# Optimization experiments

Measured on AMD Instinct MI355X. Metric: run time of the kernel, lower is better.

Reference implementation:

```python
import math
import jax, jax.numpy as jnp
import numpy as np

EMBED_DIM = 1024
ZDIM = 128
CHUNK = 2048
DSTATE = 16
DT_RANK = math.ceil(EMBED_DIM / 16)  # 64


def silu(x):
    return x * jax.nn.sigmoid(x)


def rmsnorm(x, w, eps=1e-5):
    var = jnp.mean(x * x, axis=-1, keepdims=True)
    return x * jax.lax.rsqrt(var + eps) * w


def _rotary(v, sin, cos):
    # v: (n, d) -> rotate half
    x1, x2 = jnp.split(v, 2, axis=-1)
    return jnp.concatenate([x1 * cos - x2 * sin, x2 * cos + x1 * sin], axis=-1)


def rel_pos_bias(alpha, beta, n):
    half = ZDIM // 2
    freqs = jnp.exp(jnp.arange(half, dtype=jnp.float32) * (-math.log(10000.0) / half))
    ang = jnp.arange(n, dtype=jnp.float32)[:, None] * freqs[None, :]
    sin, cos = jnp.sin(ang), jnp.cos(ang)
    a = _rotary(jnp.broadcast_to(alpha, (n, ZDIM)), sin, cos)
    b = _rotary(jnp.broadcast_to(beta, (n, ZDIM)), sin, cos)
    return jnp.einsum('mk,nk->mn', a, b)


def s6(u, xproj_w, dt_w, dt_b, A_log, D_p):
    # Mamba-style selective scan. u: (B, L, D)
    x_dbl = u @ xproj_w.T  # (B,L,dt_rank+2*N)
    dt, Bm, Cm = jnp.split(x_dbl, [DT_RANK, DT_RANK + DSTATE], axis=-1)
    dt = jax.nn.softplus(dt @ dt_w.T + dt_b)  # (B,L,D)
    A = -jnp.exp(A_log)  # (D,N)

    def step(h, inp):
        dt_t, B_t, C_t, u_t = inp  # (B,D),(B,N),(B,N),(B,D)
        dA = jnp.exp(dt_t[..., None] * A)  # (B,D,N)
        h = dA * h + (dt_t * u_t)[..., None] * B_t[:, None, :]
        y = jnp.einsum('bdn,bn->bd', h, C_t)
        return h, y

    B, L, D = u.shape
    h0 = jnp.zeros((B, D, DSTATE), u.dtype)
    xs = (dt.transpose(1, 0, 2), Bm.transpose(1, 0, 2), Cm.transpose(1, 0, 2), u.transpose(1, 0, 2))
    _, ys = jax.lax.scan(step, h0, xs)  # ys: (L,B,D)
    return ys.transpose(1, 0, 2) + u * D_p


def setup_inputs() -> dict:
    key = jax.random.key(0)
    ks = jax.random.split(key, 12)
    std = 0.02
    B, L, D = 2, 4096, EMBED_DIM
    f32 = jnp.float32
    inp = {
        'x': jax.random.normal(ks[0], (B, L, D), f32),
        'norm_w': jnp.ones((D,), f32),
        'v_w': jax.random.normal(ks[1], (D, D), f32) * std,
        'v_b': jnp.zeros((D,), f32),
        'mx_w': jax.random.normal(ks[2], (ZDIM + D + 2 * D, D), f32) * std,
        'mx_b': jnp.zeros((ZDIM + 3 * D,), f32),
        'h_w': jax.random.normal(ks[3], (D, D), f32) * std,
        'h_b': jnp.zeros((D,), f32),
        'gamma': jax.random.normal(ks[4], (2, ZDIM), f32) * std,
        'beta': jnp.zeros((2, ZDIM), f32),
        'alpha_rb': jax.random.normal(ks[5], (1, ZDIM), f32) * std,
        'beta_rb': jax.random.normal(ks[6], (1, ZDIM), f32) * std,
        'xproj_w': jax.random.normal(ks[7], (DT_RANK + 2 * DSTATE, D), f32) * std,
        'dt_w': jax.random.normal(ks[8], (D, DT_RANK), f32) * std,
        'dt_b': jnp.full((D,), -4.6, f32),  # softplus -> dt ~ 0.01
        'A_log': jnp.log(jnp.broadcast_to(jnp.arange(1, DSTATE + 1, dtype=f32), (D, DSTATE))),
        'D_p': jnp.ones((D,), f32),
    }
    return inp


def reference(x, norm_w, v_w, v_b, mx_w, mx_b, h_w, h_b, gamma, beta,
              alpha_rb, beta_rb, xproj_w, dt_w, dt_b, A_log, D_p):
    B, L, D = x.shape
    residual = x
    xn = rmsnorm(x, norm_w)
    v = silu(xn @ v_w.T + v_b)                       # (B,L,hdim)
    mx = silu(s6(xn, xproj_w, dt_w, dt_b, A_log, D_p))
    base = mx @ mx_w.T + mx_b                        # (B,L,zdim+hdim+2D)
    u, zr, hx = jnp.split(base, [D, D + ZDIM + D], axis=-1)
    u = jax.nn.sigmoid(u)
    zr = silu(zr)
    z, r = jnp.split(zr, [ZDIM], axis=-1)
    z = z[..., None, :] * gamma + beta               # (B,L,2,Z)
    q, k = z[..., 0, :], z[..., 1, :]
    c = min(CHUNK, L)
    nc = L // c
    qh = q.reshape(B, nc, c, ZDIM) * (ZDIM ** -0.5)
    kh = k.reshape(B, nc, c, ZDIM)
    vh = v.reshape(B, nc, c, D)
    bias = rel_pos_bias(alpha_rb, beta_rb, c)        # (c,c)
    mask = jnp.triu(jnp.full((c, c), -jnp.inf, jnp.float32), 1)
    qk = jnp.einsum('bnqz,bnkz->bnqk', qh, kh) + bias + mask
    attn = jax.nn.softmax(qk.astype(jnp.float32), axis=-1).astype(qk.dtype)
    h = jnp.einsum('bnqk,bnkd->bnqd', attn, vh).reshape(B, L, D)
    h = silu(hx + (h * r) @ h_w.T + h_b)
    return residual + u * (h - residual)
```

## Files before the change

### kernel.cpp

```cpp
#include <hip/hip_runtime.h>
#include <hip/hip_bf16.h>
#include <math.h>

#define EMBED 1024
#define LSEQ 4096
#define BATCH 2
#define ZD 128
#define CHUNKC 2048
#define NSTATE 16
#define DTR 64
#define XDBL_W 96
#define NSEG 64
#define TSEG 64

typedef __attribute__((ext_vector_type(8))) short bf16x8;
typedef __attribute__((ext_vector_type(4))) float f32x4;

__device__ __forceinline__ float sigmoidf_(float x){ return 1.f/(1.f+__expf(-x)); }
__device__ __forceinline__ float siluf_(float x){ return x/(1.f+__expf(-x)); }
__device__ __forceinline__ __hip_bfloat16 tobf(float x){ return __float2bfloat16(x); }
__device__ __forceinline__ float frombf(__hip_bfloat16 x){ return __bfloat162float(x); }

__device__ __forceinline__ void gload_lds16(const void* g, void* l) {
  __builtin_amdgcn_global_load_lds(
      (const __attribute__((address_space(1))) unsigned int*)g,
      (__attribute__((address_space(3))) unsigned int*)l, 16, 0, 0);
}

__global__ __launch_bounds__(256) void prep_k(
    const float* __restrict__ v_w, const float* __restrict__ xproj_w,
    const float* __restrict__ h_w, const float* __restrict__ dt_w,
    const float* __restrict__ mx_w,
    const float* __restrict__ alpha, const float* __restrict__ beta,
    __hip_bfloat16* __restrict__ wcat, __hip_bfloat16* __restrict__ hwb,
    __hip_bfloat16* __restrict__ dtwb, __hip_bfloat16* __restrict__ mxwb,
    float* __restrict__ gtab)
{
  int b = blockIdx.x, tid = threadIdx.x;
  if (b < 5440) {
    const float* s; __hip_bfloat16* d; int idx;
    if (b < 1024)      { idx = (b*256+tid)*4;        s = v_w + idx;      d = wcat + idx; }
    else if (b < 1120) { idx = ((b-1024)*256+tid)*4; s = xproj_w + idx;  d = wcat + (1<<20) + idx; }
    else if (b < 1152) { idx = ((b-1120)*256+tid)*4; s = nullptr;        d = wcat + (1<<20) + 96*1024 + idx; }
    else if (b < 2176) { idx = ((b-1152)*256+tid)*4; s = h_w + idx;      d = hwb + idx; }
    else if (b < 2240) { idx = ((b-2176)*256+tid)*4; s = dt_w + idx;     d = dtwb + idx; }
    else               { idx = ((b-2240)*256+tid)*4; s = mx_w + idx;     d = mxwb + idx; }
    if (s) {
      float4 v = *(const float4*)s;
      d[0]=tobf(v.x); d[1]=tobf(v.y); d[2]=tobf(v.z); d[3]=tobf(v.w);
    } else {
      d[0]=tobf(0.f); d[1]=tobf(0.f); d[2]=tobf(0.f); d[3]=tobf(0.f);
    }
    return;
  }
  __shared__ float P[64], Q[64], F[64];
  if (tid < 64) {
    float a1=alpha[tid], a2=alpha[64+tid], b1=beta[tid], b2=beta[64+tid];
    P[tid]=a1*b1+a2*b2;
    Q[tid]=a2*b1-a1*b2;
    F[tid]=expf(-0.14391156831f*(float)tid);
  }
  __syncthreads();
  int d = (b-5440)*256 + tid;
  if (d < CHUNKC) {
    float s=0.f;
    for (int j=0;j<64;++j){
      float th = (float)d * F[j];
      float sn, cs;
      sincosf(th, &sn, &cs);
      s += P[j]*cs - Q[j]*sn;
    }
    gtab[d]=s;
  }
}

__global__ __launch_bounds__(256) void rmsnorm_k(const float* __restrict__ x,
                                                 const float* __restrict__ w,
                                                 __hip_bfloat16* __restrict__ xnb) {
  size_t row = blockIdx.x;
  const float* px = x + row*EMBED;
  int tid = threadIdx.x;
  float4 xv = *(const float4*)(px + tid*4);
  float ss = xv.x*xv.x + xv.y*xv.y + xv.z*xv.z + xv.w*xv.w;
  #pragma unroll
  for (int off=32; off; off>>=1) ss += __shfl_down(ss, off, 64);
  __shared__ float red[4];
  if ((tid&63)==0) red[tid>>6]=ss;
  __syncthreads();
  float tot = red[0]+red[1]+red[2]+red[3];
  float scale = rsqrtf(tot*(1.f/EMBED) + 1e-5f);
  float4 wv = *(const float4*)(w + tid*4);
  __hip_bfloat16* pb = xnb + row*EMBED + tid*4;
  pb[0]=tobf(xv.x*scale*wv.x); pb[1]=tobf(xv.y*scale*wv.y);
  pb[2]=tobf(xv.z*scale*wv.z); pb[3]=tobf(xv.w*scale*wv.w);
}

template<bool FINAL>
__global__ __launch_bounds__(256) void seg_scan_k(
    const float* __restrict__ xbc,
    const __hip_bfloat16* __restrict__ dtv,
    const __hip_bfloat16* __restrict__ xnu,
    const float* __restrict__ A_log,
    const float* __restrict__ D_p,
    const float* __restrict__ segInit,
    float* __restrict__ segP,
    float* __restrict__ segH,
    __hip_bfloat16* __restrict__ mx)
{
  int bx = blockIdx.x;
  int seg = bx >> 3;
  int grp = bx & 7;
  int b = grp >> 2;
  int d = (grp & 3)*256 + threadIdx.x;
  int ch = b*EMBED + d;
  int tid = threadIdx.x;
  int tbase = seg*TSEG;

  float A[NSTATE], h[NSTATE], P[NSTATE];
  #pragma unroll
  for (int n=0;n<NSTATE;++n){
    A[n] = -__expf(A_log[(size_t)d*NSTATE+n]);
    P[n] = 1.f;
  }
  if (FINAL) {
    const float* si = segInit + ((size_t)seg*2048 + ch)*NSTATE;
    #pragma unroll
    for (int n=0;n<NSTATE;++n) h[n] = si[n];
  } else {
    #pragma unroll
    for (int n=0;n<NSTATE;++n) h[n] = 0.f;
  }
  float Dp = FINAL ? D_p[d] : 0.f;

  __shared__ float BCb[8][32];
  const float* xd = xbc + ((size_t)b*LSEQ + tbase)*32;
  const __hip_bfloat16* pdt = dtv + ((size_t)b*LSEQ + tbase)*EMBED + d;
  const __hip_bfloat16* pu  = xnu + ((size_t)b*LSEQ + tbase)*EMBED + d;
  __hip_bfloat16* pmx = mx + ((size_t)b*LSEQ + tbase)*EMBED + d;

  for (int t0=0; t0<TSEG; t0+=8) {
    __syncthreads();
    { int tt = tid>>5, jj = tid&31;
      BCb[tt][jj] = xd[(size_t)(t0+tt)*32 + jj]; }
    __syncthreads();
    #pragma unroll
    for (int tt=0; tt<8; ++tt) {
      int t = t0 + tt;
      float dtt = frombf(pdt[(size_t)t*EMBED]);
      float ut  = frombf(pu[(size_t)t*EMBED]);
      float du = dtt*ut;
      float y = 0.f;
      #pragma unroll
      for (int n=0;n<NSTATE;++n){
        float dA = __expf(dtt*A[n]);
        h[n] = dA*h[n] + du*BCb[tt][n];
        if (!FINAL) P[n] *= dA;
        if (FINAL)  y += h[n]*BCb[tt][16+n];
      }
      if (FINAL) pmx[(size_t)t*EMBED] = tobf(siluf_(y + ut*Dp));
    }
  }
  if (!FINAL) {
    float* pp = segP + ((size_t)seg*2048 + ch)*NSTATE;
    float* ph = segH + ((size_t)seg*2048 + ch)*NSTATE;
    #pragma unroll
    for (int n=0;n<NSTATE;n+=4){
      *(float4*)(pp+n) = make_float4(P[n],P[n+1],P[n+2],P[n+3]);
      *(float4*)(ph+n) = make_float4(h[n],h[n+1],h[n+2],h[n+3]);
    }
  }
}

__global__ __launch_bounds__(256) void seg_combine_k(const float* __restrict__ segP,
                                                     const float* __restrict__ segH,
                                                     float* __restrict__ segInit) {
  int idx = blockIdx.x*256 + threadIdx.x;
  float H = 0.f;
  for (int s=0; s<NSEG; ++s) {
    size_t o = (size_t)s*32768 + idx;
    float Pv = segP[o], hl = segH[o];
    segInit[o] = H;
    H = Pv*H + hl;
  }
}

__global__ __launch_bounds__(256) void softmax_k(const __hip_bfloat16* __restrict__ S,
                                                 __hip_bfloat16* __restrict__ Sb) {
  size_t row = blockIdx.x;
  const __hip_bfloat16* p = S + row*CHUNKC;
  __hip_bfloat16* po = Sb + row*CHUNKC;
  int tid = threadIdx.x;
  int r = (int)(row & (CHUNKC-1));
  int nb = (r >> 8) + 1;
  int kcl = ((r >> 7) + 1) << 7;
  float v[8];
  float m = -1e30f;
  #pragma unroll
  for (int i=0;i<8;++i){
    if (i < nb) {
      float t = frombf(p[tid + i*256]);
      v[i] = (i*256 + tid <= r) ? t : -1e30f;
    } else v[i] = -1e30f;
    m = fmaxf(m, v[i]);
  }
  #pragma unroll
  for (int off=32; off; off>>=1) m = fmaxf(m, __shfl_down(m, off, 64));
  __shared__ float red[4];
  if ((tid&63)==0) red[tid>>6]=m;
  __syncthreads();
  m = fmaxf(fmaxf(red[0],red[1]),fmaxf(red[2],red[3]));
  float s=0.f;
  #pragma unroll
  for (int i=0;i<8;++i){ v[i]=__expf(v[i]-m); s+=v[i]; }
  #pragma unroll
  for (int off=32; off; off>>=1) s += __shfl_down(s, off, 64);
  __syncthreads();
  if ((tid&63)==0) red[tid>>6]=s;
  __syncthreads();
  s = red[0]+red[1]+red[2]+red[3];
  float inv = 1.f/s;
  #pragma unroll
  for (int i=0;i<8;++i){
    int c = tid + i*256;
    if (c < kcl) po[c] = tobf(v[i]*inv);
  }
}

__global__ __launch_bounds__(256) void transpose_k(const unsigned short* __restrict__ vb,
                                                   unsigned short* __restrict__ VT) {
  __shared__ unsigned short t[64][68];
  int tid = threadIdx.x;
  int tr = tid>>4;
  int tc = (tid&15)*4;
  int c0 = blockIdx.x*64, r0 = blockIdx.y*64;
  #pragma unroll
  for (int it=0; it<4; ++it) {
    int r = it*16 + tr;
    ushort4 v = *(const ushort4*)(vb + (size_t)(r0+r)*EMBED + c0 + tc);
    t[r][tc+0]=v.x; t[r][tc+1]=v.y; t[r][tc+2]=v.z; t[r][tc+3]=v.w;
  }
  __syncthreads();
  int ch = r0 >> 11;
  int kb = r0 & 2047;
  #pragma unroll
  for (int it=0; it<4; ++it) {
    int nl = it*16 + tr;
    ushort4 o;
    o.x = t[tc+0][nl]; o.y = t[tc+1][nl]; o.z = t[tc+2][nl]; o.w = t[tc+3][nl];
    *(ushort4*)(VT + ((size_t)ch*EMBED + c0 + nl)*CHUNKC + kb + tc) = o;
  }
}

struct MEp {
  const float* bias; const float* gtab; const float* gamma; const float* beta2;
  __hip_bfloat16* ug; __hip_bfloat16* qo; __hip_bfloat16* ko; __hip_bfloat16* ro; __hip_bfloat16* hxo;
  const __hip_bfloat16* rb; const __hip_bfloat16* hxb; const __hip_bfloat16* ub;
  const float* resid; float* outp;
  __hip_bfloat16* Cb; int ldc;
  float* f32o; __hip_bfloat16* bf16o;
};

__device__ __forceinline__ void xcd_swz(int& bx, int& by) {
  const int gx = gridDim.x;
  const int nwg = gx*gridDim.y;
  const int lin = by*gx + bx;
  const int qq = nwg >> 3, rr = nwg & 7;
  const int xcd = lin & 7, pos = lin >> 3;
  const int base = (xcd < rr) ? xcd*(qq+1) : rr*(qq+1) + (xcd-rr)*qq;
  const int lg = base + pos;
  bx = lg % gx; by = lg / gx;
}

#define MBM 128
#define MBK 64

template<int EPI, bool TRIK, bool SWZ>
__global__ __launch_bounds__(256, 4) void mgemm_k(
    const __hip_bfloat16* __restrict__ A, int lda, long long sAz,
    const __hip_bfloat16* __restrict__ B, int ldb, long long sBz,
    int K, MEp ep)
{
  __shared__ __attribute__((aligned(16))) short As[MBM*MBK];
  __shared__ __attribute__((aligned(16))) short Bs[MBM*MBK];
  const int tid = threadIdx.x;
  const int wv = tid>>6, lane = tid&63;
  const int z = blockIdx.z;
  A += (size_t)z * sAz;
  B += (size_t)z * sBz;
  int bx = blockIdx.x, by = blockIdx.y;
  if constexpr (SWZ) xcd_swz(bx, by);
  const int m0 = by*MBM, n0 = bx*MBM;
  if constexpr (EPI==2) { if (n0 > m0 + (MBM-1)) return; }
  const int r8 = lane>>3, g8 = lane&7;
  const int csrc = g8 ^ r8;
  const int wr = wv>>1, wc = wv&1;
  const int fr = lane&15, qv = lane>>4;
  const int x7 = fr & 7;

  int Ktot = K;
  if constexpr (TRIK) { int km = m0 + MBM; Ktot = km < K ? km : K; }
  const int nt = Ktot / MBK;

  f32x4 acc[4][4] = {};

  const __hip_bfloat16* Ag = A + (size_t)(m0 + wv*32 + r8)*lda + csrc*8;
  const __hip_bfloat16* Bg = B + (size_t)(n0 + wv*32 + r8)*ldb + csrc*8;

  auto stage = [&](int t){
    const int k0 = t*MBK;
    short* Al = &As[wv*32*MBK];
    short* Bl = &Bs[wv*32*MBK];
    #pragma unroll
    for (int j=0;j<4;++j)
      gload_lds16(Ag + (size_t)(j*8)*lda + k0, Al + j*8*MBK);
    #pragma unroll
    for (int j=0;j<4;++j)
      gload_lds16(Bg + (size_t)(j*8)*ldb + k0, Bl + j*8*MBK);
  };

  for (int t=0; t<nt; ++t) {
    stage(t);
    __syncthreads();
    #pragma unroll
    for (int kk=0; kk<2; ++kk) {
      const int pos8 = ((kk*4 + qv) ^ x7) * 8;
      bf16x8 af[4], bfr[4];
      #pragma unroll
      for (int mi=0;mi<4;++mi)
        af[mi] = *(const bf16x8*)&As[(wr*64 + mi*16 + fr)*MBK + pos8];
      #pragma unroll
      for (int ni=0;ni<4;++ni)
        bfr[ni] = *(const bf16x8*)&Bs[(wc*64 + ni*16 + fr)*MBK + pos8];
      #pragma unroll
      for (int mi=0;mi<4;++mi)
        #pragma unroll
        for (int ni=0;ni<4;++ni)
          acc[mi][ni] = __builtin_amdgcn_mfma_f32_16x16x32_bf16(af[mi], bfr[ni], acc[mi][ni], 0,0,0);
    }
    if (t+1 < nt) __syncthreads();
  }

  const int vr = (lane>>4)*4;
  #pragma unroll
  for (int mi=0;mi<4;++mi) {
    #pragma unroll
    for (int v=0; v<4; ++v) {
      const int row = m0 + wr*64 + mi*16 + vr + v;
      #pragma unroll
      for (int ni=0;ni<4;++ni) {
        const int col = n0 + wc*64 + ni*16 + fr;
        float val = acc[mi][ni][v];
        if constexpr (EPI==1) {
          val += ep.bias[col];
          if (col < 1024) {
            ep.ug[(size_t)row*EMBED + col] = tobf(sigmoidf_(val));
          } else if (col < 1152) {
            int jj = col - 1024;
            float zz = siluf_(val);
            ep.qo[(size_t)row*ZD + jj] = tobf((zz*ep.gamma[jj] + ep.beta2[jj]) * 0.08838834764831845f);
            ep.ko[(size_t)row*ZD + jj] = tobf(zz*ep.gamma[128+jj] + ep.beta2[128+jj]);
          } else if (col < 2176) {
            ep.ro[(size_t)row*EMBED + (col-1152)] = tobf(siluf_(val));
          } else {
            ep.hxo[(size_t)row*EMBED + (col-2176)] = tobf(val);
          }
        } else if constexpr (EPI==2) {
          __hip_bfloat16* Sp = ep.Cb + (size_t)z*CHUNKC*CHUNKC;
          if (col <= row) Sp[(size_t)row*CHUNKC + col] = tobf(val + ep.gtab[row-col]);
        } else if constexpr (EPI==3) {
          size_t gr = (size_t)z*CHUNKC + row;
          ep.Cb[gr*EMBED + col] = tobf(val * frombf(ep.rb[gr*EMBED + col]));
        } else if constexpr (EPI==4) {
          float zz = val + ep.bias[col] + frombf(ep.hxb[(size_t)row*EMBED + col]);
          float hh = siluf_(zz);
          float res = ep.resid[(size_t)row*EMBED + col];
          ep.outp[(size_t)row*EMBED + col] = res + frombf(ep.ub[(size_t)row*EMBED + col])*(hh-res);
        } else if constexpr (EPI==6) {
          float zv = val + ep.bias[col];
          ep.bf16o[(size_t)row*EMBED + col] = tobf((zv > 15.f) ? zv : log1pf(__expf(zv)));
        } else {
          if (col < 1024) {
            ep.Cb[(size_t)row*ep.ldc + col] = tobf(siluf_(val + ep.bias[col]));
          } else {
            int jj = col - 1024;
            if (jj < DTR)          ep.bf16o[(size_t)row*DTR + jj] = tobf(val);
            else if (jj < XDBL_W)  ep.f32o[(size_t)row*32 + (jj - DTR)] = val;
          }
        }
      }
    }
  }
}

extern "C" void kernel_launch(void* const* d_in, const int* in_sizes, int n_in,
                              void* d_out, int out_size, void* d_ws, size_t ws_size,
                              hipStream_t stream) {
  const float* x       = (const float*)d_in[0];
  const float* norm_w  = (const float*)d_in[1];
  const float* v_w     = (const float*)d_in[2];
  const float* v_b     = (const float*)d_in[3];
  const float* mx_w    = (const float*)d_in[4];
  const float* mx_b    = (const float*)d_in[5];
  const float* h_w     = (const float*)d_in[6];
  const float* h_b     = (const float*)d_in[7];
  const float* gamma   = (const float*)d_in[8];
  const float* beta    = (const float*)d_in[9];
  const float* alpha_rb= (const float*)d_in[10];
  const float* beta_rb = (const float*)d_in[11];
  const float* xproj_w = (const float*)d_in[12];
  const float* dt_w    = (const float*)d_in[13];
  const float* dt_b    = (const float*)d_in[14];
  const float* A_log   = (const float*)d_in[15];
  const float* D_p     = (const float*)d_in[16];
  float* out = (float*)d_out;

  float* ws = (float*)d_ws;
  size_t off = 0;
  auto alloc = [&](size_t n){ float* p = ws + off; off += n; return p; };
  const size_t BL2 = (size_t)BATCH*LSEQ;

  float* sbzone  = alloc(BL2*EMBED);
  float* scratch = alloc((size_t)2*CHUNKC*CHUNKC*2);
  float* xbc     = alloc(BL2*32);
  float* gtab    = alloc(CHUNKC);
  auto balloc = [&](size_t nbf){ __hip_bfloat16* p = (__hip_bfloat16*)(ws + off); off += (nbf+1)/2; return p; };
  __hip_bfloat16* xnb   = balloc(BL2*EMBED);
  __hip_bfloat16* vbufb = balloc(BL2*EMBED);
  __hip_bfloat16* mxb   = balloc(BL2*EMBED);
  __hip_bfloat16* qb    = balloc(BL2*ZD);
  __hip_bfloat16* kb    = balloc(BL2*ZD);
  __hip_bfloat16* ugb   = balloc(BL2*EMBED);
  __hip_bfloat16* rbb   = balloc(BL2*EMBED);
  __hip_bfloat16* hxbb  = balloc(BL2*EMBED);
  __hip_bfloat16* hrb   = balloc(BL2*EMBED);
  __hip_bfloat16* xdblb = balloc(BL2*DTR);
  __hip_bfloat16* wcat  = balloc((size_t)1152*EMBED);
  __hip_bfloat16* mxwb  = balloc((size_t)3200*EMBED);
  __hip_bfloat16* hwb   = balloc((size_t)EMBED*EMBED);
  __hip_bfloat16* dtwb  = balloc((size_t)EMBED*DTR);

  __hip_bfloat16* dtbb = (__hip_bfloat16*)scratch;
  float* segP    = scratch + BL2*EMBED;
  float* segH    = segP + (size_t)NSEG*2048*NSTATE;
  float* segInit = segH + (size_t)NSEG*2048*NSTATE;
  __hip_bfloat16* S  = (__hip_bfloat16*)scratch;
  __hip_bfloat16* Sb = (__hip_bfloat16*)sbzone;
  __hip_bfloat16* VT = xnb;

  prep_k<<<5448, 256, 0, stream>>>(v_w, xproj_w, h_w, dt_w, mx_w,
                                   alpha_rb, beta_rb,
                                   wcat, hwb, dtwb, mxwb, gtab);

  rmsnorm_k<<<(int)BL2, 256, 0, stream>>>(x, norm_w, xnb);

  MEp ep;

  ep = {}; ep.bias = v_b; ep.Cb = vbufb; ep.ldc = EMBED;
  ep.f32o = xbc; ep.bf16o = xdblb;
  mgemm_k<7,false,true><<<dim3(1152/MBM, BL2/MBM), 256, 0, stream>>>(
      xnb, EMBED, 0, wcat, EMBED, 0, EMBED, ep);

  ep = {}; ep.bias = dt_b; ep.bf16o = dtbb;
  mgemm_k<6,false,true><<<dim3(EMBED/MBM, BL2/MBM), 256, 0, stream>>>(
      xdblb, DTR, 0, dtwb, DTR, 0, DTR, ep);

  seg_scan_k<false><<<NSEG*8, 256, 0, stream>>>(xbc, dtbb, xnb, A_log, D_p,
                                                nullptr, segP, segH, nullptr);
  seg_combine_k<<<128, 256, 0, stream>>>(segP, segH, segInit);
  seg_scan_k<true><<<NSEG*8, 256, 0, stream>>>(xbc, dtbb, xnb, A_log, D_p,
                                               segInit, nullptr, nullptr, mxb);

  transpose_k<<<dim3(EMBED/64, BL2/64), 256, 0, stream>>>(
      (const unsigned short*)vbufb, (unsigned short*)VT);

  ep = {}; ep.bias = mx_b; ep.gamma = gamma; ep.beta2 = beta;
  ep.ug = ugb; ep.qo = qb; ep.ko = kb; ep.ro = rbb; ep.hxo = hxbb;
  mgemm_k<1,false,true><<<dim3(3200/MBM, BL2/MBM), 256, 0, stream>>>(
      mxb, EMBED, 0, mxwb, EMBED, 0, EMBED, ep);

  ep = {}; ep.gtab = gtab; ep.Cb = S;
  mgemm_k<2,false,true><<<dim3(CHUNKC/MBM, CHUNKC/MBM, 4), 256, 0, stream>>>(
      qb, ZD, (long long)CHUNKC*ZD, kb, ZD, (long long)CHUNKC*ZD, ZD, ep);

  softmax_k<<<4*CHUNKC, 256, 0, stream>>>(S, Sb);

  ep = {}; ep.rb = rbb; ep.Cb = hrb;
  mgemm_k<3,true,true><<<dim3(EMBED/MBM, CHUNKC/MBM, 4), 256, 0, stream>>>(
      Sb, CHUNKC, (long long)CHUNKC*CHUNKC, VT, CHUNKC, (long long)EMBED*CHUNKC, CHUNKC, ep);

  ep = {}; ep.bias = h_b; ep.hxb = hxbb; ep.ub = ugb; ep.resid = x; ep.outp = out;
  mgemm_k<4,false,true><<<dim3(EMBED/MBM, BL2/MBM), 256, 0, stream>>>(
      hrb, EMBED, 0, hwb, EMBED, 0, EMBED, ep);
}
```

Baseline: 414.4 us.

## Add BK=32 GEMM variant, vectorize softmax, fold rmsnorm into prep kernel

Adds a K-tile template parameter to the MFMA GEMM. A 32-wide K tile uses half the LDS, with its own swizzle and launch bounds allowing 6 blocks per CU, and is applied to the dt, mx-projection and QK GEMMs. Softmax now gives each thread 8 contiguous bf16 values, loaded and stored as 16-byte vectors, and skips loads past the causal boundary. The rmsnorm kernel is merged into the prep kernel as extra blocks to remove a launch. Smaller K tiles mean more barriers per unit of work, which could cancel the occupancy gain.

```diff
diff --git a/kernel.cpp b/kernel.cpp
--- a/kernel.cpp
+++ b/kernel.cpp
@@ -20,6 +20,12 @@
 __device__ __forceinline__ float siluf_(float x){ return x/(1.f+__expf(-x)); }
 __device__ __forceinline__ __hip_bfloat16 tobf(float x){ return __float2bfloat16(x); }
 __device__ __forceinline__ float frombf(__hip_bfloat16 x){ return __bfloat162float(x); }
+__device__ __forceinline__ float frombits(unsigned short u){
+  __hip_bfloat16 h; *(unsigned short*)&h = u; return frombf(h);
+}
+__device__ __forceinline__ short tobits(float x){
+  __hip_bfloat16 h = tobf(x); return *(short*)&h;
+}
 
 __device__ __forceinline__ void gload_lds16(const void* g, void* l) {
   __builtin_amdgcn_global_load_lds(
@@ -32,9 +38,10 @@
     const float* __restrict__ h_w, const float* __restrict__ dt_w,
     const float* __restrict__ mx_w,
     const float* __restrict__ alpha, const float* __restrict__ beta,
+    const float* __restrict__ x, const float* __restrict__ norm_w,
     __hip_bfloat16* __restrict__ wcat, __hip_bfloat16* __restrict__ hwb,
     __hip_bfloat16* __restrict__ dtwb, __hip_bfloat16* __restrict__ mxwb,
-    float* __restrict__ gtab)
+    float* __restrict__ gtab, __hip_bfloat16* __restrict__ xnb)
 {
   int b = blockIdx.x, tid = threadIdx.x;
   if (b < 5440) {
@@ -53,33 +60,30 @@
     }
     return;
   }
-  __shared__ float P[64], Q[64], F[64];
-  if (tid < 64) {
-    float a1=alpha[tid], a2=alpha[64+tid], b1=beta[tid], b2=beta[64+tid];
-    P[tid]=a1*b1+a2*b2;
-    Q[tid]=a2*b1-a1*b2;
-    F[tid]=expf(-0.14391156831f*(float)tid);
-  }
-  __syncthreads();
-  int d = (b-5440)*256 + tid;
-  if (d < CHUNKC) {
-    float s=0.f;
-    for (int j=0;j<64;++j){
-      float th = (float)d * F[j];
-      float sn, cs;
-      sincosf(th, &sn, &cs);
-      s += P[j]*cs - Q[j]*sn;
-    }
-    gtab[d]=s;
-  }
-}
-
-__global__ __launch_bounds__(256) void rmsnorm_k(const float* __restrict__ x,
-                                                 const float* __restrict__ w,
-                                                 __hip_bfloat16* __restrict__ xnb) {
-  size_t row = blockIdx.x;
+  if (b < 5448) {
+    __shared__ float P[64], Q[64], F[64];
+    if (tid < 64) {
+      float a1=alpha[tid], a2=alpha[64+tid], b1=beta[tid], b2=beta[64+tid];
+      P[tid]=a1*b1+a2*b2;
+      Q[tid]=a2*b1-a1*b2;
+      F[tid]=expf(-0.14391156831f*(float)tid);
+    }
+    __syncthreads();
+    int d = (b-5440)*256 + tid;
+    if (d < CHUNKC) {
+      float s=0.f;
+      for (int j=0;j<64;++j){
+        float th = (float)d * F[j];
+        float sn, cs;
+        sincosf(th, &sn, &cs);
+        s += P[j]*cs - Q[j]*sn;
+      }
+      gtab[d]=s;
+    }
+    return;
+  }
+  size_t row = b - 5448;
   const float* px = x + row*EMBED;
-  int tid = threadIdx.x;
   float4 xv = *(const float4*)(px + tid*4);
   float ss = xv.x*xv.x + xv.y*xv.y + xv.z*xv.z + xv.w*xv.w;
   #pragma unroll
@@ -89,7 +93,7 @@
   __syncthreads();
   float tot = red[0]+red[1]+red[2]+red[3];
   float scale = rsqrtf(tot*(1.f/EMBED) + 1e-5f);
-  float4 wv = *(const float4*)(w + tid*4);
+  float4 wv = *(const float4*)(norm_w + tid*4);
   __hip_bfloat16* pb = xnb + row*EMBED + tid*4;
   pb[0]=tobf(xv.x*scale*wv.x); pb[1]=tobf(xv.y*scale*wv.y);
   pb[2]=tobf(xv.z*scale*wv.z); pb[3]=tobf(xv.w*scale*wv.w);
@@ -187,21 +191,25 @@
 __global__ __launch_bounds__(256) void softmax_k(const __hip_bfloat16* __restrict__ S,
                                                  __hip_bfloat16* __restrict__ Sb) {
   size_t row = blockIdx.x;
-  const __hip_bfloat16* p = S + row*CHUNKC;
-  __hip_bfloat16* po = Sb + row*CHUNKC;
+  const unsigned short* p = (const unsigned short*)(S + row*CHUNKC);
+  short* po = (short*)(Sb + row*CHUNKC);
   int tid = threadIdx.x;
   int r = (int)(row & (CHUNKC-1));
-  int nb = (r >> 8) + 1;
+  int c0 = tid*8;
   int kcl = ((r >> 7) + 1) << 7;
   float v[8];
   float m = -1e30f;
-  #pragma unroll
-  for (int i=0;i<8;++i){
-    if (i < nb) {
-      float t = frombf(p[tid + i*256]);
-      v[i] = (i*256 + tid <= r) ? t : -1e30f;
-    } else v[i] = -1e30f;
-    m = fmaxf(m, v[i]);
+  if (c0 <= r) {
+    bf16x8 raw = *(const bf16x8*)(p + c0);
+    #pragma unroll
+    for (int i=0;i<8;++i){
+      float t = frombits((unsigned short)raw[i]);
+      v[i] = (c0 + i <= r) ? t : -1e30f;
+      m = fmaxf(m, v[i]);
+    }
+  } else {
+    #pragma unroll
+    for (int i=0;i<8;++i) v[i] = -1e30f;
   }
   #pragma unroll
   for (int off=32; off; off>>=1) m = fmaxf(m, __shfl_down(m, off, 64));
@@ -219,10 +227,11 @@
   __syncthreads();
   s = red[0]+red[1]+red[2]+red[3];
   float inv = 1.f/s;
-  #pragma unroll
-  for (int i=0;i<8;++i){
-    int c = tid + i*256;
-    if (c < kcl) po[c] = tobf(v[i]*inv);
+  if (c0 < kcl) {
+    bf16x8 o;
+    #pragma unroll
+    for (int i=0;i<8;++i) o[i] = tobits(v[i]*inv);
+    *(bf16x8*)(po + c0) = o;
   }
 }
 
@@ -272,16 +281,15 @@
 }
 
 #define MBM 128
-#define MBK 64
-
-template<int EPI, bool TRIK, bool SWZ>
-__global__ __launch_bounds__(256, 4) void mgemm_k(
+
+template<int EPI, bool TRIK, bool SWZ, int BKT>
+__global__ __launch_bounds__(256, (BKT==32)?6:4) void mgemm_k(
     const __hip_bfloat16* __restrict__ A, int lda, long long sAz,
     const __hip_bfloat16* __restrict__ B, int ldb, long long sBz,
     int K, MEp ep)
 {
-  __shared__ __attribute__((aligned(16))) short As[MBM*MBK];
-  __shared__ __attribute__((aligned(16))) short Bs[MBM*MBK];
+  __shared__ __attribute__((aligned(16))) short As[MBM*BKT];
+  __shared__ __attribute__((aligned(16))) short Bs[MBM*BKT];
   const int tid = threadIdx.x;
   const int wv = tid>>6, lane = tid&63;
   const int z = blockIdx.z;
@@ -291,46 +299,81 @@
   if constexpr (SWZ) xcd_swz(bx, by);
   const int m0 = by*MBM, n0 = bx*MBM;
   if constexpr (EPI==2) { if (n0 > m0 + (MBM-1)) return; }
-  const int r8 = lane>>3, g8 = lane&7;
-  const int csrc = g8 ^ r8;
   const int wr = wv>>1, wc = wv&1;
   const int fr = lane&15, qv = lane>>4;
-  const int x7 = fr & 7;
 
   int Ktot = K;
   if constexpr (TRIK) { int km = m0 + MBM; Ktot = km < K ? km : K; }
-  const int nt = Ktot / MBK;
+  const int nt = Ktot / BKT;
 
   f32x4 acc[4][4] = {};
 
-  const __hip_bfloat16* Ag = A + (size_t)(m0 + wv*32 + r8)*lda + csrc*8;
-  const __hip_bfloat16* Bg = B + (size_t)(n0 + wv*32 + r8)*ldb + csrc*8;
+  const __hip_bfloat16* Ag;
+  const __hip_bfloat16* Bg;
+  if constexpr (BKT==64) {
+    const int r8 = lane>>3, g8 = lane&7;
+    const int csrc = g8 ^ r8;
+    Ag = A + (size_t)(m0 + wv*32 + r8)*lda + csrc*8;
+    Bg = B + (size_t)(n0 + wv*32 + r8)*ldb + csrc*8;
+  } else {
+    const int r16 = lane>>2;
+    const int csrc = (lane&3) ^ ((lane>>3)&3);
+    Ag = A + (size_t)(m0 + wv*32 + r16)*lda + csrc*8;
+    Bg = B + (size_t)(n0 + wv*32 + r16)*ldb + csrc*8;
+  }
 
   auto stage = [&](int t){
-    const int k0 = t*MBK;
-    short* Al = &As[wv*32*MBK];
-    short* Bl = &Bs[wv*32*MBK];
-    #pragma unroll
-    for (int j=0;j<4;++j)
-      gload_lds16(Ag + (size_t)(j*8)*lda + k0, Al + j*8*MBK);
-    #pragma unroll
-    for (int j=0;j<4;++j)
-      gload_lds16(Bg + (size_t)(j*8)*ldb + k0, Bl + j*8*MBK);
+    const int k0 = t*BKT;
+    short* Al = &As[wv*32*BKT];
+    short* Bl = &Bs[wv*32*BKT];
+    if constexpr (BKT==64) {
+      #pragma unroll
+      for (int j=0;j<4;++j)
+        gload_lds16(Ag + (size_t)(j*8)*lda + k0, Al + j*8*BKT);
+      #pragma unroll
+      for (int j=0;j<4;++j)
+        gload_lds16(Bg + (size_t)(j*8)*ldb + k0, Bl + j*8*BKT);
+    } else {
+      #pragma unroll
+      for (int j=0;j<2;++j)
+        gload_lds16(Ag + (size_t)(j*16)*lda + k0, Al + j*16*BKT);
+      #pragma unroll
+      for (int j=0;j<2;++j)
+        gload_lds16(Bg + (size_t)(j*16)*ldb + k0, Bl + j*16*BKT);
+    }
   };
 
   for (int t=0; t<nt; ++t) {
     stage(t);
     __syncthreads();
-    #pragma unroll
-    for (int kk=0; kk<2; ++kk) {
-      const int pos8 = ((kk*4 + qv) ^ x7) * 8;
+    if constexpr (BKT==64) {
+      const int x7 = fr & 7;
+      #pragma unroll
+      for (int kk=0; kk<2; ++kk) {
+        const int pos8 = ((kk*4 + qv) ^ x7) * 8;
+        bf16x8 af[4], bfr[4];
+        #pragma unroll
+        for (int mi=0;mi<4;++mi)
+          af[mi] = *(const bf16x8*)&As[(wr*64 + mi*16 + fr)*BKT + pos8];
+        #pragma unroll
+        for (int ni=0;ni<4;++ni)
+          bfr[ni] = *(const bf16x8*)&Bs[(wc*64 + ni*16 + fr)*BKT + pos8];
+        #pragma unroll
+        for (int mi=0;mi<4;++mi)
+          #pragma unroll
+          for (int ni=0;ni<4;++ni)
+            acc[mi][ni] = __builtin_amdgcn_mfma_f32_16x16x32_bf16(af[mi], bfr[ni], acc[mi][ni], 0,0,0);
+      }
+    } else {
+      const int x3 = (fr>>1)&3;
+      const int pos8 = (qv ^ x3) * 8;
       bf16x8 af[4], bfr[4];
       #pragma unroll
       for (int mi=0;mi<4;++mi)
-        af[mi] = *(const bf16x8*)&As[(wr*64 + mi*16 + fr)*MBK + pos8];
+        af[mi] = *(const bf16x8*)&As[(wr*64 + mi*16 + fr)*BKT + pos8];
       #pragma unroll
       for (int ni=0;ni<4;++ni)
-        bfr[ni] = *(const bf16x8*)&Bs[(wc*64 + ni*16 + fr)*MBK + pos8];
+        bfr[ni] = *(const bf16x8*)&Bs[(wc*64 + ni*16 + fr)*BKT + pos8];
       #pragma unroll
       for (int mi=0;mi<4;++mi)
         #pragma unroll
@@ -447,21 +490,19 @@
   __hip_bfloat16* Sb = (__hip_bfloat16*)sbzone;
   __hip_bfloat16* VT = xnb;
 
-  prep_k<<<5448, 256, 0, stream>>>(v_w, xproj_w, h_w, dt_w, mx_w,
-                                   alpha_rb, beta_rb,
-                                   wcat, hwb, dtwb, mxwb, gtab);
-
-  rmsnorm_k<<<(int)BL2, 256, 0, stream>>>(x, norm_w, xnb);
+  prep_k<<<5448 + (int)BL2, 256, 0, stream>>>(v_w, xproj_w, h_w, dt_w, mx_w,
+                                              alpha_rb, beta_rb, x, norm_w,
+                                              wcat, hwb, dtwb, mxwb, gtab, xnb);
 
   MEp ep;
 
   ep = {}; ep.bias = v_b; ep.Cb = vbufb; ep.ldc = EMBED;
   ep.f32o = xbc; ep.bf16o = xdblb;
-  mgemm_k<7,false,true><<<dim3(1152/MBM, BL2/MBM), 256, 0, stream>>>(
+  mgemm_k<7,false,true,64><<<dim3(1152/MBM, BL2/MBM), 256, 0, stream>>>(
       xnb, EMBED, 0, wcat, EMBED, 0, EMBED, ep);
 
   ep = {}; ep.bias = dt_b; ep.bf16o = dtbb;
-  mgemm_k<6,false,true><<<dim3(EMBED/MBM, BL2/MBM), 256, 0, stream>>>(
+  mgemm_k<6,false,true,32><<<dim3(EMBED/MBM, BL2/MBM), 256, 0, stream>>>(
       xdblb, DTR, 0, dtwb, DTR, 0, DTR, ep);
 
   seg_scan_k<false><<<NSEG*8, 256, 0, stream>>>(xbc, dtbb, xnb, A_log, D_p,
@@ -475,20 +516,20 @@
 
   ep = {}; ep.bias = mx_b; ep.gamma = gamma; ep.beta2 = beta;
   ep.ug = ugb; ep.qo = qb; ep.ko = kb; ep.ro = rbb; ep.hxo = hxbb;
-  mgemm_k<1,false,true><<<dim3(3200/MBM, BL2/MBM), 256, 0, stream>>>(
+  mgemm_k<1,false,true,32><<<dim3(3200/MBM, BL2/MBM), 256, 0, stream>>>(
       mxb, EMBED, 0, mxwb, EMBED, 0, EMBED, ep);
 
   ep = {}; ep.gtab = gtab; ep.Cb = S;
-  mgemm_k<2,false,true><<<dim3(CHUNKC/MBM, CHUNKC/MBM, 4), 256, 0, stream>>>(
+  mgemm_k<2,false,true,32><<<dim3(CHUNKC/MBM, CHUNKC/MBM, 4), 256, 0, stream>>>(
       qb, ZD, (long long)CHUNKC*ZD, kb, ZD, (long long)CHUNKC*ZD, ZD, ep);
 
   softmax_k<<<4*CHUNKC, 256, 0, stream>>>(S, Sb);
 
   ep = {}; ep.rb = rbb; ep.Cb = hrb;
-  mgemm_k<3,true,true><<<dim3(EMBED/MBM, CHUNKC/MBM, 4), 256, 0, stream>>>(
+  mgemm_k<3,true,true,64><<<dim3(EMBED/MBM, CHUNKC/MBM, 4), 256, 0, stream>>>(
       Sb, CHUNKC, (long long)CHUNKC*CHUNKC, VT, CHUNKC, (long long)EMBED*CHUNKC, CHUNKC, ep);
 
   ep = {}; ep.bias = h_b; ep.hxb = hxbb; ep.ub = ugb; ep.resid = x; ep.outp = out;
-  mgemm_k<4,false,true><<<dim3(EMBED/MBM, BL2/MBM), 256, 0, stream>>>(
+  mgemm_k<4,false,true,64><<<dim3(EMBED/MBM, BL2/MBM), 256, 0, stream>>>(
       hrb, EMBED, 0, hwb, EMBED, 0, EMBED, ep);
 }
```

Measured after the change: 766.4 us. 1.85x slower.
